# Performance work log

Measured on AMD Instinct MI355X. Metric: run time of the kernel, lower is better.

## Reference

```python
import jax, jax.numpy as jnp
import numpy as np

LOG2 = float(np.log(2.0))
CUTOFF = 10.0
NUM_G = 50
NUM_MOLS = 512


def ssp(x):
    # ShiftedSoftplus: softplus(x) - log(2)
    return jax.nn.softplus(x) - LOG2


def setup_inputs() -> dict:
    key = jax.random.key(0)
    ks = jax.random.split(key, 12)
    MOLS, ATOMS, K, H, F, G, L = NUM_MOLS, 64, 32, 128, 128, NUM_G, 6
    N = MOLS * ATOMS
    # structured radius graph: node i connects to (local+1..K) mod ATOMS in its molecule
    node = np.arange(N)
    mol = node // ATOMS
    loc = node % ATOMS
    dlt = np.arange(1, K + 1)
    src = ((loc[:, None] + dlt[None, :]) % ATOMS + mol[:, None] * ATOMS).reshape(-1)
    dst = np.repeat(node, K)
    edge_index = jnp.asarray(np.stack([src, dst]), dtype=jnp.int32)  # [2, E]
    z = jax.random.randint(ks[0], (N,), 0, 100, dtype=jnp.int32)
    # positions in a 5A cube -> all intra-molecule dists < cutoff=10
    pos = jax.random.uniform(ks[1], (N, 3), dtype=jnp.float32) * 5.0
    batch = jnp.asarray(mol, dtype=jnp.int32)

    def nrm(k, shape, scale):
        return jax.random.normal(k, shape, dtype=jnp.float32) * scale

    return dict(
        z=z, pos=pos, batch=batch, edge_index=edge_index,
        emb=nrm(ks[2], (100, H), 1.0),
        mlp_w1=nrm(ks[3], (L, G, F), 0.14),
        mlp_b1=jnp.zeros((L, F), jnp.float32),
        mlp_w2=nrm(ks[4], (L, F, F), 0.09),
        mlp_b2=jnp.zeros((L, F), jnp.float32),
        conv_w1=nrm(ks[5], (L, H, F), 0.09),
        conv_w2=nrm(ks[6], (L, F, H), 0.09),
        conv_b2=jnp.zeros((L, H), jnp.float32),
        lin_w=nrm(ks[7], (L, H, H), 0.09),
        lin_b=jnp.zeros((L, H), jnp.float32),
        out_w1=nrm(ks[8], (H, H // 2), 0.1),
        out_b1=jnp.zeros((H // 2,), jnp.float32),
        out_w2=nrm(ks[9], (H // 2, 1), 0.15),
        out_b2=jnp.zeros((1,), jnp.float32),
    )


def reference(z, pos, batch, edge_index, emb, mlp_w1, mlp_b1, mlp_w2, mlp_b2,
              conv_w1, conv_w2, conv_b2, lin_w, lin_b,
              out_w1, out_b1, out_w2, out_b2):
    N = pos.shape[0]
    src, dst = edge_index[0], edge_index[1]  # source j -> target i
    h = emb[z]                                                 # [N,H]
    d = jnp.linalg.norm(pos[dst] - pos[src], axis=-1)          # [E]
    # GaussianSmearing(start=0, stop=cutoff, num_gaussians)
    offset = jnp.linspace(0.0, CUTOFF, NUM_G)
    coeff = -0.5 / (offset[1] - offset[0]) ** 2
    edge_attr = jnp.exp(coeff * (d[:, None] - offset[None, :]) ** 2)  # [E,G]
    # cosine cutoff
    C = 0.5 * (jnp.cos(d * jnp.pi / CUTOFF) + 1.0)             # [E]
    L = mlp_w1.shape[0]
    for l in range(L):  # fixed small layer count
        # filter MLP on edge features, modulated by cutoff
        W = (ssp(edge_attr @ mlp_w1[l] + mlp_b1[l]) @ mlp_w2[l] + mlp_b2[l]) * C[:, None]  # [E,F]
        hx = h @ conv_w1[l]                                    # lin1 (no bias) [N,F]
        msg = hx[src] * W                                      # gather + modulate [E,F]
        agg = jax.ops.segment_sum(msg, dst, num_segments=N)    # scatter-add [N,F]
        v = agg @ conv_w2[l] + conv_b2[l]                      # lin2
        v = ssp(v) @ lin_w[l] + lin_b[l]                       # act + lin
        h = h + v                                              # residual
    h = ssp(h @ out_w1 + out_b1)
    h = h @ out_w2 + out_b2                                    # [N,1]
    out = jax.ops.segment_sum(h, batch, num_segments=NUM_MOLS) # per-molecule 'add' readout
    return out
```

## Files before the change

kernel.cpp:

```cpp
#include <hip/hip_runtime.h>
#include <math.h>

#define NN 32768
#define HH 128
#define GG 50
#define KK 32
#define LL 6
#define MM 512
#define TT 2048
#define TROWS 2049
#define ROWB 256

typedef _Float16 f16x8 __attribute__((ext_vector_type(8)));
typedef float    f32x4 __attribute__((ext_vector_type(4)));

__device__ __forceinline__ float ssp(float x) {
  return fmaxf(x, 0.f) + __logf(1.f + __expf(-fabsf(x))) - 0.69314718055994530942f;
}

__global__ __launch_bounds__(256)
void setup_kernel(const float* __restrict__ cw1, const float* __restrict__ cw2,
                  const float* __restrict__ lw, _Float16* __restrict__ cwT,
                  const float* __restrict__ mw1, const float* __restrict__ mw2,
                  const float* __restrict__ mb1, const float* __restrict__ mb2,
                  char* __restrict__ Vtb) {
  __shared__ float smem[2944];
  int b = blockIdx.x;
  int tid = threadIdx.x;

  if (b < 18) {
    float (*t)[33] = (float(*)[33])smem;
    int l = b / 3, m = b % 3;
    const float* w = ((m == 0) ? cw1 : (m == 1) ? cw2 : lw) + (size_t)l * 16384;
    _Float16* o = cwT + (size_t)b * 16384;
    int tx = tid & 31, ty = tid >> 5;
    for (int tj = 0; tj < 4; ++tj)
      for (int tf = 0; tf < 4; ++tf) {
        __syncthreads();
        for (int r = ty; r < 32; r += 8) t[r][tx] = w[(size_t)(tj*32 + r)*128 + tf*32 + tx];
        __syncthreads();
        for (int r = ty; r < 32; r += 8)
          o[(size_t)(tf*32 + r)*128 + tj*32 + tx] = (_Float16)t[tx][r];
      }
    return;
  }

  int bb = b - 18;
  int l  = bb / 129;
  int rb = (bb % 129) * 16;
  float (*ea)[52]  = (float(*)[52])smem;
  float (*t1)[132] = (float(*)[132])(smem + 832);

  const float DSTEP = 10.f / (float)TT;
  const float GSTEP = 10.f / 49.f;
  const float COEFF = -0.5f * 4.9f * 4.9f;
  for (int o = tid; o < 16*GG; o += 256) {
    int r = o / GG, g = o % GG;
    float d = (float)(rb + r) * DSTEP;
    float t = d - (float)g * GSTEP;
    ea[r][g] = __expf(COEFF * t * t);
  }
  __syncthreads();

  int f = tid & 127, rg = (tid >> 7) * 8;
  {
    float acc[8];
    float bv = mb1[l*128 + f];
    #pragma unroll
    for (int r = 0; r < 8; ++r) acc[r] = bv;
    for (int g = 0; g < GG; ++g) {
      float wv = mw1[(size_t)(l*GG + g)*128 + f];
      #pragma unroll
      for (int r = 0; r < 8; ++r) acc[r] = fmaf(ea[rg + r][g], wv, acc[r]);
    }
    #pragma unroll
    for (int r = 0; r < 8; ++r) t1[rg + r][f] = ssp(acc[r]);
  }
  __syncthreads();
  {
    float acc[8];
    float bv = mb2[l*128 + f];
    #pragma unroll
    for (int r = 0; r < 8; ++r) acc[r] = bv;
    for (int j = 0; j < 128; ++j) {
      float wv = mw2[(size_t)(l*128 + j)*128 + f];
      #pragma unroll
      for (int r = 0; r < 8; ++r) acc[r] = fmaf(t1[rg + r][j], wv, acc[r]);
    }
    #pragma unroll
    for (int r = 0; r < 8; ++r) {
      int rr = rb + rg + r;
      if (rr <= TT) {
        float d = (float)rr * DSTEP;
        float Cc = 0.5f * (__cosf(d * 0.31415926535897931f) + 1.f);
        _Float16* row = (_Float16*)(Vtb + ((size_t)l*TROWS + rr) * ROWB);
        row[f] = (_Float16)(acc[r] * Cc);
      }
    }
  }
}

__device__ __forceinline__ void wave_gemm(const _Float16 (*__restrict__ A)[136],
                                          const _Float16* __restrict__ B,
                                          int c, int q, int n0, f32x4* res) {
  f16x8 bf[4];
  #pragma unroll
  for (int kk = 0; kk < 4; ++kk)
    bf[kk] = *(const f16x8*)&B[(size_t)(n0 + c)*128 + kk*32 + q*8];
  #pragma unroll
  for (int m = 0; m < 4; ++m) {
    f32x4 a = {0.f, 0.f, 0.f, 0.f};
    #pragma unroll
    for (int kk = 0; kk < 4; ++kk) {
      f16x8 av = *(const f16x8*)&A[m*16 + c][kk*32 + q*8];
      a = __builtin_amdgcn_mfma_f32_16x16x32_f16(av, bf[kk], a, 0, 0, 0);
    }
    res[m] = a;
  }
}

__global__ __launch_bounds__(512, 4)
void mega_kernel(const int* __restrict__ z, const float* __restrict__ pos,
                 const float* __restrict__ emb,
                 const _Float16* __restrict__ cwT,
                 const float* __restrict__ cb2, const float* __restrict__ lb,
                 const char* __restrict__ Vtb,
                 const float* __restrict__ ow1, const float* __restrict__ ob1,
                 const float* __restrict__ ow2, const float* __restrict__ ob2,
                 float* __restrict__ out) {
  __shared__ _Float16     hcur[64][136];
  __shared__ _Float16     sb[64][136];
  __shared__ _Float16     hxs[64][136];
  __shared__ float        posL[64][4];
  __shared__ unsigned int edata[64*33];
  __shared__ float        red[512];

  int tid = threadIdx.x;
  int wave = tid >> 6, lane = tid & 63;
  int q = lane >> 4, c = lane & 15;
  int n0 = wave * 16;
  int mol = blockIdx.x, gbase = mol * 64;

  if (tid < 192) posL[tid / 3][tid % 3] = pos[(size_t)gbase*3 + tid];
  for (int o = tid; o < 64*64; o += 512) {
    int n = o >> 6, p2 = (o & 63) * 2;
    float2 ev = *(const float2*)&emb[(size_t)z[gbase + n]*128 + p2];
    hcur[n][p2]     = (_Float16)ev.x;
    hcur[n][p2 + 1] = (_Float16)ev.y;
  }
  __syncthreads();

  for (int e = tid; e < 2048; e += 512) {
    int n = e >> 5, k = e & 31;
    int s = (n + k + 1) & 63;
    float dx = posL[n][0] - posL[s][0];
    float dy = posL[n][1] - posL[s][1];
    float dz = posL[n][2] - posL[s][2];
    float d = sqrtf(dx*dx + dy*dy + dz*dz);
    int idx = (int)(d * ((float)TT / 10.f) + 0.5f);
    edata[n*33 + k] = (unsigned int)idx << 8;
  }
  __syncthreads();

  int en = tid >> 3, ej = tid & 7;
  int f0 = ej * 8;

  for (int l = 0; l < LL; ++l) {
    {
      f32x4 res[4];
      wave_gemm(hcur, cwT + (size_t)(l*3 + 0)*16384, c, q, n0, res);
      #pragma unroll
      for (int m = 0; m < 4; ++m)
        #pragma unroll
        for (int r = 0; r < 4; ++r)
          hxs[m*16 + q*4 + r][n0 + c] = (_Float16)res[m][r];
    }
    __syncthreads();

    f16x8 accA0 = {0,0,0,0,0,0,0,0}, accA1 = accA0;
    f16x8 accB0 = accA0, accB1 = accA0;
    const char* Vl = Vtb + (size_t)l * TROWS * ROWB + f0*2;
    #pragma unroll 4
    for (int k = 0; k < KK; ++k) {
      unsigned int off = edata[en*33 + k];
      int s = (en + k + 1) & 63;
      const char* p = Vl + off;
      f16x8 va = *(const f16x8*)p;
      f16x8 vb = *(const f16x8*)(p + 128);
      f16x8 ha = *(const f16x8*)&hxs[s][f0];
      f16x8 hb = *(const f16x8*)&hxs[s][f0 + 64];
      if (k & 1) { accA1 = ha * va + accA1; accB1 = hb * vb + accB1; }
      else       { accA0 = ha * va + accA0; accB0 = hb * vb + accB0; }
    }
    *(f16x8*)&sb[en][f0]      = accA0 + accA1;
    *(f16x8*)&sb[en][f0 + 64] = accB0 + accB1;
    __syncthreads();

    {
      f32x4 vres[4];
      wave_gemm(sb, cwT + (size_t)(l*3 + 1)*16384, c, q, n0, vres);
      float b2v = cb2[l*128 + n0 + c];
      #pragma unroll
      for (int m = 0; m < 4; ++m)
        #pragma unroll
        for (int r = 0; r < 4; ++r)
          hxs[m*16 + q*4 + r][n0 + c] = (_Float16)ssp(vres[m][r] + b2v);
    }
    __syncthreads();

    {
      f32x4 res[4];
      wave_gemm(hxs, cwT + (size_t)(l*3 + 2)*16384, c, q, n0, res);
      float lbv = lb[l*128 + n0 + c];
      #pragma unroll
      for (int m = 0; m < 4; ++m)
        #pragma unroll
        for (int r = 0; r < 4; ++r) {
          int row = m*16 + q*4 + r;
          float h = (float)hcur[row][n0 + c];
          hcur[row][n0 + c] = (_Float16)(h + res[m][r] + lbv);
        }
    }
    __syncthreads();
  }

  float partial = 0.f;
  for (int o = tid; o < 64*64; o += 512) {
    int n = o >> 6, fo = o & 63;
    float acc = ob1[fo];
    for (int j = 0; j < 128; j += 8) {
      f16x8 h8 = *(const f16x8*)&hcur[n][j];
      #pragma unroll
      for (int jj = 0; jj < 8; ++jj)
        acc = fmaf((float)h8[jj], ow1[(j + jj)*64 + fo], acc);
    }
    partial += ssp(acc) * ow2[fo];
  }
  red[tid] = partial;
  __syncthreads();
  for (int s = 256; s > 0; s >>= 1) {
    if (tid < s) red[tid] += red[tid + s];
    __syncthreads();
  }
  if (tid == 0) out[mol] = red[0] + 64.f * ob2[0];
}

extern "C" void kernel_launch(void* const* d_in, const int* in_sizes, int n_in,
                              void* d_out, int out_size, void* d_ws, size_t ws_size,
                              hipStream_t stream) {
  const int*   z       = (const int*)d_in[0];
  const float* pos     = (const float*)d_in[1];
  const float* emb     = (const float*)d_in[4];
  const float* mlp_w1  = (const float*)d_in[5];
  const float* mlp_b1  = (const float*)d_in[6];
  const float* mlp_w2  = (const float*)d_in[7];
  const float* mlp_b2  = (const float*)d_in[8];
  const float* conv_w1 = (const float*)d_in[9];
  const float* conv_w2 = (const float*)d_in[10];
  const float* conv_b2 = (const float*)d_in[11];
  const float* lin_w   = (const float*)d_in[12];
  const float* lin_b   = (const float*)d_in[13];
  const float* out_w1  = (const float*)d_in[14];
  const float* out_b1  = (const float*)d_in[15];
  const float* out_w2  = (const float*)d_in[16];
  const float* out_b2  = (const float*)d_in[17];

  char*     Vtb = (char*)d_ws;
  _Float16* cwT = (_Float16*)(Vtb + (size_t)LL*TROWS*ROWB);

  setup_kernel<<<18 + LL*129, 256, 0, stream>>>(conv_w1, conv_w2, lin_w, cwT,
      mlp_w1, mlp_w2, mlp_b1, mlp_b2, Vtb);
  mega_kernel<<<MM, 512, 0, stream>>>(z, pos, emb, cwT, conv_b2, lin_b,
      Vtb, out_w1, out_b1, out_w2, out_b2, (float*)d_out);
}
```

Before: 232.3 us.

## Compute filter-table MLP with split-fp16 MFMA instead of scalar FMA

The setup stage that tabulates the filter MLP over distance bins now runs on MFMA matrix instructions. Each fp32 value is split into a high and a low fp16 part and combined with three MFMAs to keep near-fp32 accuracy. The mlp weights are pre-transposed and split by a new small kernel, which adds a launch. The goal is to cut the scalar FMA cost of the 6x2049x128 table build, at the price of an extra kernel and triple-precision MFMA work.

```diff
diff --git a/kernel.cpp b/kernel.cpp
--- a/kernel.cpp
+++ b/kernel.cpp
@@ -19,21 +19,21 @@
 }
 
 __global__ __launch_bounds__(256)
-void setup_kernel(const float* __restrict__ cw1, const float* __restrict__ cw2,
-                  const float* __restrict__ lw, _Float16* __restrict__ cwT,
-                  const float* __restrict__ mw1, const float* __restrict__ mw2,
-                  const float* __restrict__ mb1, const float* __restrict__ mb2,
-                  char* __restrict__ Vtb) {
-  __shared__ float smem[2944];
+void setup_a(const float* __restrict__ cw1, const float* __restrict__ cw2,
+             const float* __restrict__ lw, _Float16* __restrict__ cwT,
+             const float* __restrict__ mw1, const float* __restrict__ mw2,
+             _Float16* __restrict__ w1hT, _Float16* __restrict__ w1lT,
+             _Float16* __restrict__ w2hT, _Float16* __restrict__ w2lT) {
+  __shared__ float smem[1056];
+  float (*t)[33] = (float(*)[33])smem;
   int b = blockIdx.x;
   int tid = threadIdx.x;
+  int tx = tid & 31, ty = tid >> 5;
 
   if (b < 18) {
-    float (*t)[33] = (float(*)[33])smem;
     int l = b / 3, m = b % 3;
     const float* w = ((m == 0) ? cw1 : (m == 1) ? cw2 : lw) + (size_t)l * 16384;
     _Float16* o = cwT + (size_t)b * 16384;
-    int tx = tid & 31, ty = tid >> 5;
     for (int tj = 0; tj < 4; ++tj)
       for (int tf = 0; tf < 4; ++tf) {
         __syncthreads();
@@ -44,57 +44,122 @@
       }
     return;
   }
-
-  int bb = b - 18;
-  int l  = bb / 129;
-  int rb = (bb % 129) * 16;
-  float (*ea)[52]  = (float(*)[52])smem;
-  float (*t1)[132] = (float(*)[132])(smem + 832);
+  if (b < 24) {
+    int l = b - 18;
+    const float* w = mw2 + (size_t)l * 16384;
+    for (int tj = 0; tj < 4; ++tj)
+      for (int tf = 0; tf < 4; ++tf) {
+        __syncthreads();
+        for (int r = ty; r < 32; r += 8) t[r][tx] = w[(size_t)(tj*32 + r)*128 + tf*32 + tx];
+        __syncthreads();
+        for (int r = ty; r < 32; r += 8) {
+          float v = t[tx][r];
+          _Float16 h = (_Float16)v;
+          size_t oi = ((size_t)l*128 + tf*32 + r)*128 + tj*32 + tx;
+          w2hT[oi] = h;
+          w2lT[oi] = (_Float16)(v - (float)h);
+        }
+      }
+    return;
+  }
+  {
+    int l = b - 24;
+    const float* w = mw1 + (size_t)l * (GG*128);
+    for (int tj = 0; tj < 2; ++tj)
+      for (int tf = 0; tf < 4; ++tf) {
+        __syncthreads();
+        for (int r = ty; r < 32; r += 8) {
+          int g = tj*32 + r;
+          t[r][tx] = (g < GG) ? w[(size_t)g*128 + tf*32 + tx] : 0.f;
+        }
+        __syncthreads();
+        for (int r = ty; r < 32; r += 8) {
+          float v = t[tx][r];
+          _Float16 h = (_Float16)v;
+          size_t oi = ((size_t)l*128 + tf*32 + r)*64 + tj*32 + tx;
+          w1hT[oi] = h;
+          w1lT[oi] = (_Float16)(v - (float)h);
+        }
+      }
+  }
+}
+
+__global__ __launch_bounds__(256)
+void setup_b(const float* __restrict__ mb1, const float* __restrict__ mb2,
+             const _Float16* __restrict__ w1hT, const _Float16* __restrict__ w1lT,
+             const _Float16* __restrict__ w2hT, const _Float16* __restrict__ w2lT,
+             char* __restrict__ Vtb) {
+  __shared__ _Float16 eah[16][72], eal[16][72];
+  __shared__ _Float16 t1h[16][136], t1l[16][136];
+
+  int tid = threadIdx.x;
+  int l  = blockIdx.x / 129;
+  int rb = (blockIdx.x % 129) * 16;
+  int wave = tid >> 6, lane = tid & 63;
+  int q = lane >> 4, c = lane & 15;
 
   const float DSTEP = 10.f / (float)TT;
   const float GSTEP = 10.f / 49.f;
   const float COEFF = -0.5f * 4.9f * 4.9f;
-  for (int o = tid; o < 16*GG; o += 256) {
-    int r = o / GG, g = o % GG;
+
+  for (int o = tid; o < 16*64; o += 256) {
+    int r = o >> 6, g = o & 63;
     float d = (float)(rb + r) * DSTEP;
-    float t = d - (float)g * GSTEP;
-    ea[r][g] = __expf(COEFF * t * t);
-  }
-  __syncthreads();
-
-  int f = tid & 127, rg = (tid >> 7) * 8;
-  {
-    float acc[8];
-    float bv = mb1[l*128 + f];
-    #pragma unroll
-    for (int r = 0; r < 8; ++r) acc[r] = bv;
-    for (int g = 0; g < GG; ++g) {
-      float wv = mw1[(size_t)(l*GG + g)*128 + f];
-      #pragma unroll
-      for (int r = 0; r < 8; ++r) acc[r] = fmaf(ea[rg + r][g], wv, acc[r]);
-    }
-    #pragma unroll
-    for (int r = 0; r < 8; ++r) t1[rg + r][f] = ssp(acc[r]);
-  }
-  __syncthreads();
-  {
-    float acc[8];
-    float bv = mb2[l*128 + f];
-    #pragma unroll
-    for (int r = 0; r < 8; ++r) acc[r] = bv;
-    for (int j = 0; j < 128; ++j) {
-      float wv = mw2[(size_t)(l*128 + j)*128 + f];
-      #pragma unroll
-      for (int r = 0; r < 8; ++r) acc[r] = fmaf(t1[rg + r][j], wv, acc[r]);
-    }
-    #pragma unroll
-    for (int r = 0; r < 8; ++r) {
-      int rr = rb + rg + r;
+    float tt = d - (float)g * GSTEP;
+    float v = (g < GG) ? __expf(COEFF * tt * tt) : 0.f;
+    _Float16 h = (_Float16)v;
+    eah[r][g] = h;
+    eal[r][g] = (_Float16)(v - (float)h);
+  }
+  __syncthreads();
+
+  #pragma unroll
+  for (int tI = 0; tI < 2; ++tI) {
+    int col = (wave*2 + tI)*16 + c;
+    f32x4 a = {0.f, 0.f, 0.f, 0.f};
+    #pragma unroll
+    for (int kk = 0; kk < 2; ++kk) {
+      f16x8 bh = *(const f16x8*)&w1hT[((size_t)l*128 + col)*64 + kk*32 + q*8];
+      f16x8 bl = *(const f16x8*)&w1lT[((size_t)l*128 + col)*64 + kk*32 + q*8];
+      f16x8 ah = *(const f16x8*)&eah[c][kk*32 + q*8];
+      f16x8 al = *(const f16x8*)&eal[c][kk*32 + q*8];
+      a = __builtin_amdgcn_mfma_f32_16x16x32_f16(ah, bh, a, 0, 0, 0);
+      a = __builtin_amdgcn_mfma_f32_16x16x32_f16(ah, bl, a, 0, 0, 0);
+      a = __builtin_amdgcn_mfma_f32_16x16x32_f16(al, bh, a, 0, 0, 0);
+    }
+    float bv = mb1[l*128 + col];
+    #pragma unroll
+    for (int r = 0; r < 4; ++r) {
+      float v = ssp(a[r] + bv);
+      _Float16 h = (_Float16)v;
+      t1h[q*4 + r][col] = h;
+      t1l[q*4 + r][col] = (_Float16)(v - (float)h);
+    }
+  }
+  __syncthreads();
+
+  #pragma unroll
+  for (int tI = 0; tI < 2; ++tI) {
+    int col = (wave*2 + tI)*16 + c;
+    f32x4 a = {0.f, 0.f, 0.f, 0.f};
+    #pragma unroll
+    for (int kk = 0; kk < 4; ++kk) {
+      f16x8 bh = *(const f16x8*)&w2hT[((size_t)l*128 + col)*128 + kk*32 + q*8];
+      f16x8 bl = *(const f16x8*)&w2lT[((size_t)l*128 + col)*128 + kk*32 + q*8];
+      f16x8 ah = *(const f16x8*)&t1h[c][kk*32 + q*8];
+      f16x8 al = *(const f16x8*)&t1l[c][kk*32 + q*8];
+      a = __builtin_amdgcn_mfma_f32_16x16x32_f16(ah, bh, a, 0, 0, 0);
+      a = __builtin_amdgcn_mfma_f32_16x16x32_f16(ah, bl, a, 0, 0, 0);
+      a = __builtin_amdgcn_mfma_f32_16x16x32_f16(al, bh, a, 0, 0, 0);
+    }
+    float bv = mb2[l*128 + col];
+    #pragma unroll
+    for (int r = 0; r < 4; ++r) {
+      int rr = rb + q*4 + r;
       if (rr <= TT) {
         float d = (float)rr * DSTEP;
         float Cc = 0.5f * (__cosf(d * 0.31415926535897931f) + 1.f);
-        _Float16* row = (_Float16*)(Vtb + ((size_t)l*TROWS + rr) * ROWB);
-        row[f] = (_Float16)(acc[r] * Cc);
+        ((_Float16*)(Vtb + ((size_t)l*TROWS + rr) * ROWB))[col] = (_Float16)((a[r] + bv) * Cc);
       }
     }
   }
@@ -265,11 +330,16 @@
   const float* out_w2  = (const float*)d_in[16];
   const float* out_b2  = (const float*)d_in[17];
 
-  char*     Vtb = (char*)d_ws;
-  _Float16* cwT = (_Float16*)(Vtb + (size_t)LL*TROWS*ROWB);
-
-  setup_kernel<<<18 + LL*129, 256, 0, stream>>>(conv_w1, conv_w2, lin_w, cwT,
-      mlp_w1, mlp_w2, mlp_b1, mlp_b2, Vtb);
+  char*     Vtb  = (char*)d_ws;
+  _Float16* cwT  = (_Float16*)(Vtb + (size_t)LL*TROWS*ROWB);
+  _Float16* w2hT = cwT  + (size_t)18*16384;
+  _Float16* w2lT = w2hT + (size_t)LL*16384;
+  _Float16* w1hT = w2lT + (size_t)LL*16384;
+  _Float16* w1lT = w1hT + (size_t)LL*8192;
+
+  setup_a<<<30, 256, 0, stream>>>(conv_w1, conv_w2, lin_w, cwT,
+      mlp_w1, mlp_w2, w1hT, w1lT, w2hT, w2lT);
+  setup_b<<<LL*129, 256, 0, stream>>>(mlp_b1, mlp_b2, w1hT, w1lT, w2hT, w2lT, Vtb);
   mega_kernel<<<MM, 512, 0, stream>>>(z, pos, emb, cwT, conv_b2, lin_b,
       Vtb, out_w1, out_b1, out_w2, out_b2, (float*)d_out);
 }
```

Result: slower. 242.1 us (+4.2%).
